# Kernel optimization log

Hardware: AMD Instinct MI355X
Metric: run time of the kernel (lower is better)

The kernel has to match this reference:

```python
import jax, jax.numpy as jnp
import numpy as np


def conv1x1(x, w, b):
    # x: [B,C,H,W], w: [O,C], b: [O] -> [B,O,H,W]
    return jnp.einsum('bchw,oc->bohw', x, w) + b[None, :, None, None]


def setup_inputs() -> dict:
    key = jax.random.key(0)
    ks = jax.random.split(key, 8)
    B, C, H, W = 16, 256, 64, 64
    Cq = C // 8
    x = jax.random.normal(ks[0], (B, C, H, W), dtype=jnp.float32)
    wq = jax.random.normal(ks[1], (Cq, C), dtype=jnp.float32) * (2.0 / C) ** 0.5
    bq = jnp.zeros((Cq,), dtype=jnp.float32)
    wk = jax.random.normal(ks[2], (Cq, C), dtype=jnp.float32) * (2.0 / C) ** 0.5
    bk = jnp.zeros((Cq,), dtype=jnp.float32)
    wv = jax.random.normal(ks[3], (C, C), dtype=jnp.float32) * (2.0 / C) ** 0.5
    bv = jnp.zeros((C,), dtype=jnp.float32)
    gamma = jax.random.normal(ks[4], (1,), dtype=jnp.float32) * 0.1
    return {'x': x, 'wq': wq, 'bq': bq, 'wk': wk, 'bk': bk, 'wv': wv, 'bv': bv, 'gamma': gamma}


def reference(x, wq, bq, wk, bk, wv, bv, gamma):
    B, C, H, W = x.shape
    bH = B // 4
    bW = B // 4  # requires bH*bW == B, i.e. B == 16
    q = conv1x1(x, wq, bq)   # [B, C/8, H, W]
    k = conv1x1(x, wk, bk)   # [B, C/8, H, W]
    v = conv1x1(x, wv, bv)   # [B, C, H, W]
    # batch index b -> grid (h = b // bW, w = b % bW); token feature = flat map
    qg = q.reshape(bH, bW, -1)  # [bH, bW, Dq]
    kg = k.reshape(bH, bW, -1)
    vg = v.reshape(bH, bW, -1)  # [bH, bW, Dv]
    # column ('H') attention with -inf diagonal, row ('W') attention
    eH = jnp.einsum('hwd,gwd->hwg', qg, kg)  # [bH, bW, bH]
    eye = jnp.eye(bH, dtype=bool)[:, None, :]  # mask h == h'
    eH = jnp.where(eye, -jnp.inf, eH)
    eW = jnp.einsum('hwd,hgd->hwg', qg, kg)  # [bH, bW, bW]
    att = jax.nn.softmax(jnp.concatenate([eH, eW], axis=-1), axis=-1)
    aH, aW = att[..., :bH], att[..., bH:]
    oH = jnp.einsum('hwg,gwd->hwd', aH, vg)  # attend down the column
    oW = jnp.einsum('hwg,hgd->hwd', aW, vg)  # attend along the row
    out = (oH + oW).reshape(B, C, H, W)
    return gamma[0] * out + x
```

## Files before the change

### kernel.cpp

```cpp
#include <hip/hip_runtime.h>

#define HW_  4096
#define DQK  131072
#define DV   1048576

using bf16x8 = __attribute__((ext_vector_type(8))) __bf16;
using f32x4  = __attribute__((ext_vector_type(4))) float;

static __device__ __forceinline__ unsigned short f2bf(float f) {
    union { float f; unsigned u; } v; v.f = f;
    unsigned r = v.u + 0x7FFFu + ((v.u >> 16) & 1u);
    return (unsigned short)(r >> 16);
}
static __device__ __forceinline__ float bf2f(unsigned short h) {
    union { unsigned u; float f; } v; v.u = ((unsigned)h) << 16;
    return v.f;
}

static __device__ __forceinline__ f32x4 xp4(f32x4 v, bool p0, bool p1) {
    float e01 = p0 ? v[0] : v[1];
    float r01 = __shfl_xor(e01, 1);
    float x0 = p0 ? r01 : v[0];
    float x1 = p0 ? v[1] : r01;
    float e23 = p0 ? v[2] : v[3];
    float r23 = __shfl_xor(e23, 1);
    float x2 = p0 ? r23 : v[2];
    float x3 = p0 ? v[3] : r23;
    float eA = p1 ? x0 : x2;
    float rA = __shfl_xor(eA, 2);
    float w0 = p1 ? rA : x0;
    float w2 = p1 ? x2 : rA;
    float eB = p1 ? x1 : x3;
    float rB = __shfl_xor(eB, 2);
    float w1 = p1 ? rB : x1;
    float w3 = p1 ? x3 : rB;
    return (f32x4){w0, w1, w2, w3};
}

__global__ __launch_bounds__(256) void k_pack(const float* wq, const float* wk, const float* wv,
                                              unsigned short* WhF, unsigned short* WlF, unsigned short* WvF) {
    int idx = blockIdx.x * 256 + threadIdx.x;
    if (idx < 16384) {
        int i = idx;
        int mt = i >> 12, cg = (i >> 7) & 31, ml = (i >> 3) & 15, cl = i & 7;
        int m = mt * 16 + ml, c = cg * 8 + cl;
        float f = (m < 32) ? wq[m * 256 + c] : wk[(m - 32) * 256 + c];
        unsigned short hi = f2bf(f);
        WhF[i] = hi;
        WlF[i] = f2bf(f - bf2f(hi));
    } else {
        int i = idx - 16384;
        int mt = i >> 12, kt = (i >> 7) & 31, lr = (i >> 3) & 15, j = i & 7;
        int m = mt * 16 + lr, c = kt * 8 + j;
        WvF[i] = f2bf(wv[m * 256 + c]);
    }
}

__global__ __launch_bounds__(256) void k_gemm_qk(const unsigned short* __restrict__ WhF,
                                                 const unsigned short* __restrict__ WlF,
                                                 const float* __restrict__ x,
                                                 const float* __restrict__ bq, const float* __restrict__ bk,
                                                 float* __restrict__ QF, float* __restrict__ KF) {
    int b  = blockIdx.y;
    int n0 = blockIdx.x * 64;
    int t = threadIdx.x;
    int lane = t & 63, wid = t >> 6;
    int wm = wid & 1, wn = wid >> 1;
    int lr = lane & 15, kg = lane >> 4;

    const float* xb = x + (size_t)b * DV;
    const unsigned short* Ah0 = WhF + (size_t)(wm * 2) * 4096 + lane * 8;
    const unsigned short* Al0 = WlF + (size_t)(wm * 2) * 4096 + lane * 8;

    f32x4 acc[2][2];
    for (int mi = 0; mi < 2; mi++)
        for (int ni = 0; ni < 2; ni++) acc[mi][ni] = (f32x4){0.f, 0.f, 0.f, 0.f};

    for (int kk = 0; kk < 8; kk++) {
        bf16x8 ah[2], al[2];
        for (int mi = 0; mi < 2; mi++) {
            ah[mi] = *(const bf16x8*)(Ah0 + (size_t)mi * 4096 + kk * 512);
            al[mi] = *(const bf16x8*)(Al0 + (size_t)mi * 4096 + kk * 512);
        }
        bf16x8 bh[2], bl[2];
        int cbase = kk * 32 + kg * 8;
        for (int ni = 0; ni < 2; ni++) {
            const float* xp = xb + (size_t)cbase * HW_ + n0 + wn * 32 + ni * 16 + lr;
            #pragma unroll
            for (int j = 0; j < 8; j++) {
                float v = xp[(size_t)j * HW_];
                __bf16 h = (__bf16)v;
                bh[ni][j] = h;
                bl[ni][j] = (__bf16)(v - (float)h);
            }
        }
        for (int mi = 0; mi < 2; mi++)
            for (int ni = 0; ni < 2; ni++) {
                acc[mi][ni] = __builtin_amdgcn_mfma_f32_16x16x32_bf16(ah[mi], bh[ni], acc[mi][ni], 0, 0, 0);
                acc[mi][ni] = __builtin_amdgcn_mfma_f32_16x16x32_bf16(ah[mi], bl[ni], acc[mi][ni], 0, 0, 0);
                acc[mi][ni] = __builtin_amdgcn_mfma_f32_16x16x32_bf16(al[mi], bh[ni], acc[mi][ni], 0, 0, 0);
            }
    }

    float* dst = (wm == 0) ? QF : KF;
    const float* bias = (wm == 0) ? bq : bk;
    for (int mi = 0; mi < 2; mi++) {
        int mq0 = mi * 16 + kg * 4;
        for (int i = 0; i < 4; i++) {
            int mq = mq0 + i;
            float bs = bias[mq];
            for (int ni = 0; ni < 2; ni++) {
                int n = n0 + wn * 32 + ni * 16 + lr;
                dst[(size_t)b * DQK + (size_t)mq * HW_ + n] = acc[mi][ni][i] + bs;
            }
        }
    }
}

__global__ __launch_bounds__(256) void k_scores2(const float* __restrict__ QF, const float* __restrict__ KF,
                                                 float* __restrict__ Sp) {
    __shared__ float Ql[16][520], Kl[16][520];
    int s = blockIdx.x;
    int m = s >> 3, off = (s & 7) * 512;
    int t = threadIdx.x;
    for (int b = 0; b < 16; b++) {
        const float* qs = QF + (size_t)b * DQK + (size_t)m * HW_ + off;
        const float* ks = KF + (size_t)b * DQK + (size_t)m * HW_ + off;
        Ql[b][t]       = qs[t];
        Ql[b][t + 256] = qs[t + 256];
        Kl[b][t]       = ks[t];
        Kl[b][t + 256] = ks[t + 256];
    }
    __syncthreads();
    int p = t >> 1, h = t & 1;
    int b = p >> 3, j = p & 7;
    int hb = b >> 2, wb = b & 3;
    int bp = (j < 4) ? (j * 4 + wb) : (hb * 4 + (j - 4));
    const f32x4* q4 = (const f32x4*)&Ql[b][h * 256];
    const f32x4* k4 = (const f32x4*)&Kl[bp][h * 256];
    f32x4 a4 = (f32x4){0.f, 0.f, 0.f, 0.f};
    for (int i = 0; i < 64; i++) a4 += q4[i] * k4[i];
    float sres = a4[0] + a4[1] + a4[2] + a4[3];
    sres += __shfl_xor(sres, 1);
    if (h == 0) Sp[(size_t)p * 256 + s] = sres;
}

__global__ void k_softmax2(const float* __restrict__ Sp, const float* __restrict__ gamma,
                           float* __restrict__ Mm) {
    __shared__ float SS[128];
    int t = threadIdx.x;
    const f32x4* s4 = (const f32x4*)(Sp + (size_t)t * 256);
    f32x4 a = (f32x4){0.f, 0.f, 0.f, 0.f};
    for (int i = 0; i < 64; i++) a += s4[i];
    SS[t] = a[0] + a[1] + a[2] + a[3];
    __syncthreads();
    if (t < 16) {
        int b = t, h = b >> 2, w = b & 3;
        float e[8];
        for (int j = 0; j < 8; j++) e[j] = SS[b * 8 + j];
        e[h] = -INFINITY;
        float mx = e[0];
        for (int j = 1; j < 8; j++) mx = fmaxf(mx, e[j]);
        float aa[8], sum = 0.f;
        for (int j = 0; j < 8; j++) { aa[j] = expf(e[j] - mx); sum += aa[j]; }
        float inv = 1.0f / sum;
        float g = gamma[0];
        float row[16];
        for (int c = 0; c < 16; c++) row[c] = 0.f;
        for (int gg = 0; gg < 4; gg++) if (gg != h) row[gg * 4 + w] += aa[gg] * inv;
        for (int gg = 0; gg < 4; gg++) row[h * 4 + gg] += aa[4 + gg] * inv;
        for (int c = 0; c < 16; c++) Mm[b * 16 + c] = row[c] * g;
        Mm[256 + b] = g;
    }
}

__global__ __launch_bounds__(256) void k_mix(const float* __restrict__ Mm, const float* __restrict__ x,
                                             unsigned short* __restrict__ Xm) {
    __shared__ float Ms[256];
    __shared__ unsigned short T[16][32][36];
    using u16x4 = __attribute__((ext_vector_type(4))) unsigned short;
    int t = threadIdx.x;
    int p0 = blockIdx.x * 32, c0 = blockIdx.y * 32;
    Ms[t] = Mm[t];

    int c_l = t >> 3, p4 = t & 7;
    f32x4 in4[16];
    for (int bp = 0; bp < 16; bp++)
        in4[bp] = *(const f32x4*)(x + (size_t)bp * DV + (size_t)(c0 + c_l) * HW_ + p0 + p4 * 4);
    __syncthreads();
    for (int b = 0; b < 16; b++) {
        int h = b >> 2, w = b & 3;
        f32x4 acc = (f32x4){0.f, 0.f, 0.f, 0.f};
        #pragma unroll
        for (int g = 0; g < 4; g++) {
            if (g != h) acc += Ms[b * 16 + g * 4 + w] * in4[g * 4 + w];
            acc += Ms[b * 16 + h * 4 + g] * in4[h * 4 + g];
        }
        for (int e = 0; e < 4; e++) T[b][p4 * 4 + e][c_l] = f2bf(acc[e]);
    }
    __syncthreads();
    int p_l = t >> 3, cq = t & 7;
    int p = p0 + p_l;
    int c = c0 + cq * 4;
    size_t dst = (size_t)(p >> 4) * 4096 + (size_t)(c >> 3) * 128 + (p & 15) * 8 + (c & 7);
    for (int b = 0; b < 16; b++) {
        u16x4 v = *(const u16x4*)&T[b][p_l][cq * 4];
        *(u16x4*)(Xm + (size_t)b * DV + dst) = v;
    }
}

__global__ __launch_bounds__(512) void k_gemm_v_res(const unsigned short* __restrict__ WvF,
                                                    const unsigned short* __restrict__ XmF,
                                                    const float* __restrict__ bv,
                                                    const float* __restrict__ MmRs,
                                                    const float* __restrict__ x,
                                                    float* __restrict__ out) {
    int b  = blockIdx.y;
    int n0 = blockIdx.x * 64;
    int t = threadIdx.x;
    int lane = t & 63, wid = t >> 6;
    int wm = wid >> 1, wn = wid & 1;
    int lr = lane & 15, kg = lane >> 4;

    const unsigned short* Bb = XmF + (size_t)b * DV + (size_t)(blockIdx.x * 4 + wn * 2) * 4096 + lane * 8;
    const unsigned short* Ab = WvF + (size_t)(wm * 4) * 4096 + lane * 8;

    bf16x8 bfr[8][2];
    #pragma unroll
    for (int kk = 0; kk < 8; kk++)
        #pragma unroll
        for (int ni = 0; ni < 2; ni++)
            bfr[kk][ni] = *(const bf16x8*)(Bb + (size_t)ni * 4096 + kk * 512);

    f32x4 acc[4][2];
    #pragma unroll
    for (int mi = 0; mi < 4; mi++)
        for (int ni = 0; ni < 2; ni++) acc[mi][ni] = (f32x4){0.f, 0.f, 0.f, 0.f};

    bf16x8 a[4], an[4];
    #pragma unroll
    for (int mi = 0; mi < 4; mi++) a[mi] = *(const bf16x8*)(Ab + (size_t)mi * 4096);
    #pragma unroll
    for (int kk = 0; kk < 8; kk++) {
        if (kk < 7) {
            #pragma unroll
            for (int mi = 0; mi < 4; mi++)
                an[mi] = *(const bf16x8*)(Ab + (size_t)mi * 4096 + (kk + 1) * 512);
        }
        #pragma unroll
        for (int mi = 0; mi < 4; mi++)
            #pragma unroll
            for (int ni = 0; ni < 2; ni++)
                acc[mi][ni] = __builtin_amdgcn_mfma_f32_16x16x32_bf16(a[mi], bfr[kk][ni], acc[mi][ni], 0, 0, 0);
        #pragma unroll
        for (int mi = 0; mi < 4; mi++) a[mi] = an[mi];
    }

    float rs = MmRs[256 + b];
    bool p0 = (lane & 1) != 0, p1 = (lane & 2) != 0;
    #pragma unroll
    for (int mi = 0; mi < 4; mi++) {
        int mrow0 = wm * 64 + mi * 16 + kg * 4;
        f32x4 bvv = *(const f32x4*)(bv + mrow0);
        int mrow = mrow0 + (lane & 3);
        #pragma unroll
        for (int ni = 0; ni < 2; ni++) {
            f32x4 mo = acc[mi][ni] + rs * bvv;
            f32x4 w4 = xp4(mo, p0, p1);
            int nq = n0 + wn * 32 + ni * 16 + (lr >> 2) * 4;
            size_t g = (size_t)b * DV + (size_t)mrow * HW_ + nq;
            f32x4 rr = *(const f32x4*)(x + g);
            __builtin_nontemporal_store(w4 + rr, (f32x4*)(out + g));
        }
    }
}

extern "C" void kernel_launch(void* const* d_in, const int* in_sizes, int n_in,
                              void* d_out, int out_size, void* d_ws, size_t ws_size,
                              hipStream_t stream) {
    (void)in_sizes; (void)n_in; (void)out_size; (void)ws_size;
    const float* x     = (const float*)d_in[0];
    const float* wq    = (const float*)d_in[1];
    const float* bq    = (const float*)d_in[2];
    const float* wk    = (const float*)d_in[3];
    const float* bk    = (const float*)d_in[4];
    const float* wv    = (const float*)d_in[5];
    const float* bv    = (const float*)d_in[6];
    const float* gamma = (const float*)d_in[7];

    char* ws = (char*)d_ws;
    unsigned short* WhF = (unsigned short*)(ws + 0);
    unsigned short* WlF = (unsigned short*)(ws + 32768);
    unsigned short* WvF = (unsigned short*)(ws + 65536);
    float*          QF  = (float*)(ws + 196608);
    float*          KF  = (float*)(ws + 8585216);
    unsigned short* Xm  = (unsigned short*)(ws + 16973824);
    float*          Sp  = (float*)(ws + 16973824);
    float*          Mm  = (float*)(ws + 0);
    float*          vo  = (float*)d_out;

    k_pack       <<<320, 256, 0, stream>>>(wq, wk, wv, WhF, WlF, WvF);
    k_gemm_qk    <<<dim3(64, 16), 256, 0, stream>>>(WhF, WlF, x, bq, bk, QF, KF);
    k_scores2    <<<256, 256, 0, stream>>>(QF, KF, Sp);
    k_softmax2   <<<1, 128, 0, stream>>>(Sp, gamma, Mm);
    k_mix        <<<dim3(128, 8), 256, 0, stream>>>(Mm, x, Xm);
    k_gemm_v_res <<<dim3(64, 16), 512, 0, stream>>>(WvF, Xm, bv, Mm, x, vo);
}
```

Baseline: 91.72 us.

## Coalesce stores in Q/K, mix, and V-GEMM epilogues via layout and LDS staging

The Q/K projection now writes each block's results as contiguous fragment-ordered vector stores, and the scores kernel reads contiguous 512-element slices to match. This works because the per-slice dot product does not depend on element order. The mix kernel writes 8-wide bf16 vectors instead of 4-wide ones, using a padded, aligned LDS tile. The V-GEMM epilogue stages its accumulators through a 256x68 float LDS buffer so that full 64-column rows of out and x are read and written coalesced, replacing the lane-shuffle transpose. The cost is extra shared memory and a block-wide sync in the GEMM, which may lower occupancy.

```diff
diff --git a/kernel.cpp b/kernel.cpp
--- a/kernel.cpp
+++ b/kernel.cpp
@@ -6,6 +6,7 @@
 
 using bf16x8 = __attribute__((ext_vector_type(8))) __bf16;
 using f32x4  = __attribute__((ext_vector_type(4))) float;
+using u16x8  = __attribute__((ext_vector_type(8))) unsigned short;
 
 static __device__ __forceinline__ unsigned short f2bf(float f) {
     union { float f; unsigned u; } v; v.f = f;
@@ -15,26 +16,6 @@
 static __device__ __forceinline__ float bf2f(unsigned short h) {
     union { unsigned u; float f; } v; v.u = ((unsigned)h) << 16;
     return v.f;
-}
-
-static __device__ __forceinline__ f32x4 xp4(f32x4 v, bool p0, bool p1) {
-    float e01 = p0 ? v[0] : v[1];
-    float r01 = __shfl_xor(e01, 1);
-    float x0 = p0 ? r01 : v[0];
-    float x1 = p0 ? v[1] : r01;
-    float e23 = p0 ? v[2] : v[3];
-    float r23 = __shfl_xor(e23, 1);
-    float x2 = p0 ? r23 : v[2];
-    float x3 = p0 ? v[3] : r23;
-    float eA = p1 ? x0 : x2;
-    float rA = __shfl_xor(eA, 2);
-    float w0 = p1 ? rA : x0;
-    float w2 = p1 ? x2 : rA;
-    float eB = p1 ? x1 : x3;
-    float rB = __shfl_xor(eB, 2);
-    float w1 = p1 ? rB : x1;
-    float w3 = p1 ? x3 : rB;
-    return (f32x4){w0, w1, w2, w3};
 }
 
 __global__ __launch_bounds__(256) void k_pack(const float* wq, const float* wk, const float* wv,
@@ -104,15 +85,13 @@
 
     float* dst = (wm == 0) ? QF : KF;
     const float* bias = (wm == 0) ? bq : bk;
+    size_t base = (size_t)b * DQK + (size_t)blockIdx.x * 2048;
     for (int mi = 0; mi < 2; mi++) {
-        int mq0 = mi * 16 + kg * 4;
-        for (int i = 0; i < 4; i++) {
-            int mq = mq0 + i;
-            float bs = bias[mq];
-            for (int ni = 0; ni < 2; ni++) {
-                int n = n0 + wn * 32 + ni * 16 + lr;
-                dst[(size_t)b * DQK + (size_t)mq * HW_ + n] = acc[mi][ni][i] + bs;
-            }
+        f32x4 bvv = *(const f32x4*)(bias + mi * 16 + kg * 4);
+        for (int ni = 0; ni < 2; ni++) {
+            int slot = (wn * 2 + ni) * 2 + mi;
+            f32x4 v = acc[mi][ni] + bvv;
+            *(f32x4*)(dst + base + slot * 256 + lane * 4) = v;
         }
     }
 }
@@ -121,11 +100,11 @@
                                                  float* __restrict__ Sp) {
     __shared__ float Ql[16][520], Kl[16][520];
     int s = blockIdx.x;
-    int m = s >> 3, off = (s & 7) * 512;
+    size_t off = (size_t)s * 512;
     int t = threadIdx.x;
     for (int b = 0; b < 16; b++) {
-        const float* qs = QF + (size_t)b * DQK + (size_t)m * HW_ + off;
-        const float* ks = KF + (size_t)b * DQK + (size_t)m * HW_ + off;
+        const float* qs = QF + (size_t)b * DQK + off;
+        const float* ks = KF + (size_t)b * DQK + off;
         Ql[b][t]       = qs[t];
         Ql[b][t + 256] = qs[t + 256];
         Kl[b][t]       = ks[t];
@@ -177,8 +156,7 @@
 __global__ __launch_bounds__(256) void k_mix(const float* __restrict__ Mm, const float* __restrict__ x,
                                              unsigned short* __restrict__ Xm) {
     __shared__ float Ms[256];
-    __shared__ unsigned short T[16][32][36];
-    using u16x4 = __attribute__((ext_vector_type(4))) unsigned short;
+    __shared__ __align__(16) unsigned short T[16][32][40];
     int t = threadIdx.x;
     int p0 = blockIdx.x * 32, c0 = blockIdx.y * 32;
     Ms[t] = Mm[t];
@@ -199,13 +177,15 @@
         for (int e = 0; e < 4; e++) T[b][p4 * 4 + e][c_l] = f2bf(acc[e]);
     }
     __syncthreads();
-    int p_l = t >> 3, cq = t & 7;
+    int p_l = t & 31, co = (t >> 5) & 3, bh = t >> 7;
     int p = p0 + p_l;
-    int c = c0 + cq * 4;
-    size_t dst = (size_t)(p >> 4) * 4096 + (size_t)(c >> 3) * 128 + (p & 15) * 8 + (c & 7);
-    for (int b = 0; b < 16; b++) {
-        u16x4 v = *(const u16x4*)&T[b][p_l][cq * 4];
-        *(u16x4*)(Xm + (size_t)b * DV + dst) = v;
+    int c = c0 + co * 8;
+    size_t dst = (size_t)(p >> 4) * 4096 + (size_t)(c >> 3) * 128 + (p & 15) * 8;
+    #pragma unroll
+    for (int bi = 0; bi < 8; bi++) {
+        int b = bh * 8 + bi;
+        u16x8 v = *(const u16x8*)&T[b][p_l][co * 8];
+        *(u16x8*)(Xm + (size_t)b * DV + dst) = v;
     }
 }
 
@@ -215,6 +195,7 @@
                                                     const float* __restrict__ MmRs,
                                                     const float* __restrict__ x,
                                                     float* __restrict__ out) {
+    __shared__ __align__(16) float LD[256][68];
     int b  = blockIdx.y;
     int n0 = blockIdx.x * 64;
     int t = threadIdx.x;
@@ -257,21 +238,27 @@
     }
 
     float rs = MmRs[256 + b];
-    bool p0 = (lane & 1) != 0, p1 = (lane & 2) != 0;
     #pragma unroll
     for (int mi = 0; mi < 4; mi++) {
         int mrow0 = wm * 64 + mi * 16 + kg * 4;
         f32x4 bvv = *(const f32x4*)(bv + mrow0);
-        int mrow = mrow0 + (lane & 3);
         #pragma unroll
         for (int ni = 0; ni < 2; ni++) {
             f32x4 mo = acc[mi][ni] + rs * bvv;
-            f32x4 w4 = xp4(mo, p0, p1);
-            int nq = n0 + wn * 32 + ni * 16 + (lr >> 2) * 4;
-            size_t g = (size_t)b * DV + (size_t)mrow * HW_ + nq;
-            f32x4 rr = *(const f32x4*)(x + g);
-            __builtin_nontemporal_store(w4 + rr, (f32x4*)(out + g));
-        }
+            int ncol = wn * 32 + ni * 16 + lr;
+            #pragma unroll
+            for (int i = 0; i < 4; i++) LD[mrow0 + i][ncol] = mo[i];
+        }
+    }
+    __syncthreads();
+    #pragma unroll
+    for (int ps = 0; ps < 8; ps++) {
+        int row = wid * 32 + ps * 4 + (lane >> 4);
+        int nc  = (lane & 15) * 4;
+        f32x4 o = *(const f32x4*)&LD[row][nc];
+        size_t g = (size_t)b * DV + (size_t)row * HW_ + n0 + nc;
+        f32x4 rr = *(const f32x4*)(x + g);
+        __builtin_nontemporal_store(o + rr, (f32x4*)(out + g));
     }
 }
 
```

New measurement: 85.95 us. -6.3%, faster.
